# Kernel tuning notes

Hardware: AMD Instinct MI355X
Metric: run time of the kernel (lower is better)

The kernel has to match this reference:

```python
import jax, jax.numpy as jnp
import numpy as np

B, S, D = 2, 2048, 1024
N_HEADS = 16
PAT_HEADS = N_HEADS // 4          # MultiheadAttention num_heads = 4
HEAD_DIM = D // PAT_HEADS         # 256
SPARSITY_RATIO = 0.1
MEMORY_PRESSURE = 0.5
NEG_INF = -1e9


def setup_inputs() -> dict:
    key = jax.random.key(0)
    ks = jax.random.split(key, 16)
    sd = 1.0 / np.sqrt(D)
    sh = 1.0 / np.sqrt(D // 4)
    inp = {
        "q": jax.random.normal(ks[0], (B, S, D), jnp.float32),
        "k": jax.random.normal(ks[1], (B, S, D), jnp.float32),
        "v": jax.random.normal(ks[2], (B, S, D), jnp.float32),
        # sparsity predictor: Linear(D, D//4) -> ReLU -> Linear(D//4, 1) -> Sigmoid
        "w1": jax.random.uniform(ks[3], (D, D // 4), jnp.float32, -sd, sd),
        "b1": jax.random.uniform(ks[4], (D // 4,), jnp.float32, -sd, sd),
        "w2": jax.random.uniform(ks[5], (D // 4, 1), jnp.float32, -sh, sh),
        "b2": jax.random.uniform(ks[6], (1,), jnp.float32, -sh, sh),
        # MultiheadAttention in_proj (split) + out_proj, stored [in, out]
        "wq": jax.random.uniform(ks[7], (D, D), jnp.float32, -sd, sd),
        "bq": jnp.zeros((D,), jnp.float32),
        "wk": jax.random.uniform(ks[8], (D, D), jnp.float32, -sd, sd),
        "bk": jnp.zeros((D,), jnp.float32),
        "wv": jax.random.uniform(ks[9], (D, D), jnp.float32, -sd, sd),
        "bv": jnp.zeros((D,), jnp.float32),
        "wo": jax.random.uniform(ks[10], (D, D), jnp.float32, -sd, sd),
        "bo": jnp.zeros((D,), jnp.float32),
    }
    return inp


def reference(q, k, v, w1, b1, w2, b2, wq, bq, wk, bk, wv, bv, wo, bo):
    # learned importance scores -> boolean mask of active tokens
    h = jax.nn.relu(q @ w1 + b1)                       # [B,S,D//4]
    scores = jax.nn.sigmoid(h @ w2 + b2)[..., 0]       # [B,S]
    threshold = SPARSITY_RATIO * (1.0 + MEMORY_PRESSURE)
    mask = scores > threshold                          # [B,S] bool

    # original module flattens all active tokens across batch into ONE
    # sequence and runs MHA over that subset; we express the identical math
    # with a fixed-shape masked attention over the flattened [B*S] tokens.
    N = B * S
    mf = mask.reshape(N)                               # [N]
    qf = q.reshape(N, D)
    kf = k.reshape(N, D)
    vf = v.reshape(N, D)

    qp = (qf @ wq + bq).reshape(N, PAT_HEADS, HEAD_DIM)
    kp = (kf @ wk + bk).reshape(N, PAT_HEADS, HEAD_DIM)
    vp = (vf @ wv + bv).reshape(N, PAT_HEADS, HEAD_DIM)

    scale = 1.0 / np.sqrt(HEAD_DIM)
    logits = jnp.einsum("nhd,mhd->hnm", qp * scale, kp)   # [H,N,N]
    logits = jnp.where(mf[None, None, :], logits, NEG_INF)  # only active keys
    attn = jax.nn.softmax(logits, axis=-1)
    ctx = jnp.einsum("hnm,mhd->nhd", attn, vp).reshape(N, D)
    out = ctx @ wo + bo                                 # [N,D]

    # scatter back: inactive query positions stay zero
    out = jnp.where(mf[:, None], out, 0.0)
    return out.reshape(B, S, D)
```

## Files before the change

### kernel.cpp

```cpp
#include <hip/hip_runtime.h>
#include <hip/hip_bf16.h>
#include <math.h>

typedef __bf16 bf16x8 __attribute__((ext_vector_type(8)));
typedef __bf16 bf16x4 __attribute__((ext_vector_type(4)));
typedef float  f32x4  __attribute__((ext_vector_type(4)));
typedef float  f32x16 __attribute__((ext_vector_type(16)));
typedef short  s16x8  __attribute__((ext_vector_type(8)));

#define N_TOK  4096
#define DMODEL 1024
#define NHEAD  4
#define DHEAD  256

__device__ __forceinline__ f32x4 mfma16x16(bf16x8 a, bf16x8 b, f32x4 c) {
    return __builtin_amdgcn_mfma_f32_16x16x32_bf16(a, b, c, 0, 0, 0);
}
__device__ __forceinline__ f32x16 mfma32(bf16x8 a, bf16x8 b, f32x16 c) {
    return __builtin_amdgcn_mfma_f32_32x32x16_bf16(a, b, c, 0, 0, 0);
}
__device__ __forceinline__ unsigned cvtpk(float lo, float hi) {
    unsigned r;
    asm("v_cvt_pk_bf16_f32 %0, %1, %2" : "=v"(r) : "v"(lo), "v"(hi));
    return r;
}

__device__ __forceinline__ void gload_lds16(const void* gsrc, void* ldst) {
    __builtin_amdgcn_global_load_lds(
        (const __attribute__((address_space(1))) void*)gsrc,
        (__attribute__((address_space(3))) void*)ldst, 16, 0, 0);
}

struct CvtArgs { const float* src[3]; __bf16* dst[3]; };
__global__ __launch_bounds__(256)
void cvt_bf16_kernel(CvtArgs a)
{
    const float* in = a.src[blockIdx.y];
    __bf16* out = a.dst[blockIdx.y];
    size_t i8 = ((size_t)blockIdx.x * 256 + threadIdx.x) * 8;
    f32x4 t0 = *(const f32x4*)(in + i8);
    f32x4 t1 = *(const f32x4*)(in + i8 + 4);
    bf16x8 b;
    #pragma unroll
    for (int j = 0; j < 4; ++j) { b[j] = (__bf16)t0[j]; b[j + 4] = (__bf16)t1[j]; }
    *(bf16x8*)(out + i8) = b;
}

__device__ __forceinline__ void transposew_body(const float* __restrict__ in,
                                                __bf16* __restrict__ out, int C)
{
    __shared__ __align__(16) __bf16 tile[64 * 72];
    const int tid = threadIdx.x;
    const int r0 = blockIdx.x * 64;
    const int c0 = blockIdx.y * 64;
    if (c0 >= C) return;
    #pragma unroll
    for (int it = 0; it < 4; ++it) {
        int i = tid + it * 256;
        int row = i >> 4, c4 = i & 15;
        f32x4 v = *(const f32x4*)(in + (size_t)(r0 + row) * C + c0 + c4 * 4);
        #pragma unroll
        for (int j = 0; j < 4; ++j)
            tile[(c4 * 4 + j) * 72 + row] = (__bf16)v[j];
    }
    __syncthreads();
    #pragma unroll
    for (int it = 0; it < 2; ++it) {
        int i = tid + it * 256;
        int col = i >> 3, ch = i & 7;
        s16x8 v = *(const s16x8*)(&tile[col * 72 + ch * 8]);
        *(s16x8*)((short*)out + (size_t)(c0 + col) * 1024 + r0 + ch * 8) = v;
    }
}

__global__ __launch_bounds__(256)
void transposew_kernel(const float* __restrict__ in, __bf16* __restrict__ out, int C)
{
    transposew_body(in, out, C);
}

struct TWArgs { const float* src[4]; __bf16* dst[4]; int C[4]; };
__global__ __launch_bounds__(256)
void transposew_batch_kernel(TWArgs a)
{
    int z = blockIdx.z;
    transposew_body(a.src[z], a.dst[z], a.C[z]);
}

struct GemmDesc {
    const __bf16* A; const __bf16* B; const float* bias; __bf16* C;
    int lda, ldb, ldc, gx, nblocks, relu, biasrow; float scale;
};
struct FusedArgs { GemmDesc d[4]; };

__global__ __launch_bounds__(256, 2)
void gemm_fused(FusedArgs fa)
{
    __shared__ __align__(16) short As[2][128 * 64];
    __shared__ __align__(16) short Bs[2][128 * 64];

    int b = blockIdx.x, z = 0;
    while (b >= fa.d[z].nblocks) { b -= fa.d[z].nblocks; ++z; }
    const GemmDesc D = fa.d[z];
    const int m0 = (b % D.gx) * 128;
    const int n0 = (b / D.gx) * 128;

    const int tid  = threadIdx.x;
    const int lane = tid & 63;
    const int wv   = tid >> 6;
    const int c16  = lane & 15;
    const int quad = lane >> 4;
    const int swz  = c16 & 7;
    const int wr   = wv >> 1;
    const int wc   = wv & 1;

    f32x4 acc[4][4];
    #pragma unroll
    for (int i = 0; i < 4; ++i)
        #pragma unroll
        for (int j = 0; j < 4; ++j)
            acc[i][j] = (f32x4){0.f, 0.f, 0.f, 0.f};

    const int sRow = lane >> 3;
    const int sCh  = (lane & 7) ^ (sRow & 7);

    auto issue = [&](short* Abuf, short* Bbuf, int k0) {
        #pragma unroll
        for (int g = 0; g < 4; ++g) {
            int row = 32 * wv + 8 * g + sRow;
            const char* src = (const char*)(D.A + (size_t)(m0 + row) * D.lda + k0) + sCh * 16;
            gload_lds16(src, (char*)Abuf + (32 * wv + 8 * g) * 128);
        }
        #pragma unroll
        for (int g = 0; g < 4; ++g) {
            int row = 32 * wv + 8 * g + sRow;
            const char* src = (const char*)(D.B + (size_t)(n0 + row) * D.ldb + k0) + sCh * 16;
            gload_lds16(src, (char*)Bbuf + (32 * wv + 8 * g) * 128);
        }
    };
    auto compute = [&](const short* Abuf, const short* Bbuf) {
        __builtin_amdgcn_s_setprio(1);
        #pragma unroll
        for (int ks = 0; ks < 2; ++ks) {
            bf16x8 af[4], bfr[4];
            int slot = ((ks * 4 + quad) ^ swz) * 16;
            #pragma unroll
            for (int t = 0; t < 4; ++t)
                af[t] = *(const bf16x8*)((const char*)Abuf + (wr * 64 + t * 16 + c16) * 128 + slot);
            #pragma unroll
            for (int t = 0; t < 4; ++t)
                bfr[t] = *(const bf16x8*)((const char*)Bbuf + (wc * 64 + t * 16 + c16) * 128 + slot);
            #pragma unroll
            for (int tm = 0; tm < 4; ++tm)
                #pragma unroll
                for (int tn = 0; tn < 4; ++tn)
                    acc[tm][tn] = mfma16x16(af[tm], bfr[tn], acc[tm][tn]);
        }
        __builtin_amdgcn_s_setprio(0);
    };

    issue(As[0], Bs[0], 0);
    __syncthreads();

    #pragma unroll 1
    for (int t = 0; t < 16; t += 2) {
        if (t + 1 < 16) issue(As[1], Bs[1], (t + 1) << 6);
        compute(As[0], Bs[0]);
        __syncthreads();
        if (t + 2 < 16) issue(As[0], Bs[0], (t + 2) << 6);
        compute(As[1], Bs[1]);
        __syncthreads();
    }

    #pragma unroll
    for (int tm = 0; tm < 4; ++tm) {
        #pragma unroll
        for (int rr = 0; rr < 4; ++rr) {
            int row = m0 + wr * 64 + tm * 16 + quad * 4 + rr;
            float rbv = D.biasrow ? D.bias[row] : 0.0f;
            #pragma unroll
            for (int tn = 0; tn < 4; ++tn) {
                int col = n0 + wc * 64 + tn * 16 + c16;
                float bb = D.biasrow ? rbv : D.bias[col];
                float val = (acc[tm][tn][rr] + bb) * D.scale;
                if (D.relu) val = fmaxf(val, 0.0f);
                D.C[(size_t)row * D.ldc + col] = (__bf16)val;
            }
        }
    }
}

template<typename OutT, bool BIASROW>
__global__ __launch_bounds__(256, 2)
void gemm_bt64(const __bf16* __restrict__ A, int lda,
               const __bf16* __restrict__ B, int ldb,
               const float* __restrict__ bias,
               OutT* __restrict__ C, int ldc,
               float scale, int relu, const float* __restrict__ rowmask, int K)
{
    __shared__ __align__(16) short As[2][128 * 64];
    __shared__ __align__(16) short Bs[2][64 * 64];
    const int tid  = threadIdx.x;
    const int lane = tid & 63;
    const int wv   = tid >> 6;
    const int c16  = lane & 15;
    const int quad = lane >> 4;
    const int swz  = c16 & 7;
    const int wr   = wv >> 1;
    const int wc   = wv & 1;
    const int m0 = blockIdx.x * 128;
    const int n0 = blockIdx.y * 64;

    f32x4 acc[4][2];
    #pragma unroll
    for (int i = 0; i < 4; ++i)
        #pragma unroll
        for (int j = 0; j < 2; ++j)
            acc[i][j] = (f32x4){0.f, 0.f, 0.f, 0.f};

    const int sRow = lane >> 3;
    const int sCh  = (lane & 7) ^ (sRow & 7);

    auto issue = [&](short* Abuf, short* Bbuf, int k0) {
        #pragma unroll
        for (int g = 0; g < 4; ++g) {
            int row = 32 * wv + 8 * g + sRow;
            const char* src = (const char*)(A + (size_t)(m0 + row) * lda + k0) + sCh * 16;
            gload_lds16(src, (char*)Abuf + (32 * wv + 8 * g) * 128);
        }
        #pragma unroll
        for (int g = 0; g < 2; ++g) {
            int row = 16 * wv + 8 * g + sRow;
            const char* src = (const char*)(B + (size_t)(n0 + row) * ldb + k0) + sCh * 16;
            gload_lds16(src, (char*)Bbuf + (16 * wv + 8 * g) * 128);
        }
    };
    auto compute = [&](const short* Abuf, const short* Bbuf) {
        __builtin_amdgcn_s_setprio(1);
        #pragma unroll
        for (int ks = 0; ks < 2; ++ks) {
            bf16x8 af[4], bfr[2];
            int slot = ((ks * 4 + quad) ^ swz) * 16;
            #pragma unroll
            for (int t = 0; t < 4; ++t)
                af[t] = *(const bf16x8*)((const char*)Abuf + (wr * 64 + t * 16 + c16) * 128 + slot);
            #pragma unroll
            for (int t = 0; t < 2; ++t)
                bfr[t] = *(const bf16x8*)((const char*)Bbuf + (wc * 32 + t * 16 + c16) * 128 + slot);
            #pragma unroll
            for (int tm = 0; tm < 4; ++tm)
                #pragma unroll
                for (int tn = 0; tn < 2; ++tn)
                    acc[tm][tn] = mfma16x16(af[tm], bfr[tn], acc[tm][tn]);
        }
        __builtin_amdgcn_s_setprio(0);
    };

    const int nt = K >> 6;
    issue(As[0], Bs[0], 0);
    __syncthreads();

    #pragma unroll 1
    for (int t = 0; t < nt; t += 2) {
        if (t + 1 < nt) issue(As[1], Bs[1], (t + 1) << 6);
        compute(As[0], Bs[0]);
        __syncthreads();
        if (t + 1 < nt) {
            if (t + 2 < nt) issue(As[0], Bs[0], (t + 2) << 6);
            compute(As[1], Bs[1]);
            __syncthreads();
        }
    }

    #pragma unroll
    for (int tm = 0; tm < 4; ++tm) {
        #pragma unroll
        for (int rr = 0; rr < 4; ++rr) {
            int row = m0 + wr * 64 + tm * 16 + quad * 4 + rr;
            float mk = rowmask ? rowmask[row] : 1.0f;
            float rbv = BIASROW ? bias[row] : 0.0f;
            #pragma unroll
            for (int tn = 0; tn < 2; ++tn) {
                int col = n0 + wc * 32 + tn * 16 + c16;
                float b = BIASROW ? rbv : bias[col];
                float val = (acc[tm][tn][rr] + b) * scale;
                if (relu) val = fmaxf(val, 0.0f);
                val *= mk;
                C[(size_t)row * ldc + col] = (OutT)val;
            }
        }
    }
}

__global__ void score_mask_kernel(const __bf16* __restrict__ h,
                                  const float* __restrict__ w2,
                                  const float* __restrict__ b2,
                                  float* __restrict__ maskf)
{
    int lane = threadIdx.x & 63;
    int tok  = blockIdx.x * 4 + (threadIdx.x >> 6);
    const __bf16* hr = h + (size_t)tok * 256;
    float s = 0.f;
    #pragma unroll
    for (int j = 0; j < 4; ++j) {
        int c = j * 64 + lane;
        s += (float)hr[c] * w2[c];
    }
    #pragma unroll
    for (int o = 1; o < 64; o <<= 1) s += __shfl_xor(s, o);
    if (lane == 0) {
        float x = s + b2[0];
        maskf[tok] = (x > -1.7346010553881064f) ? 1.0f : 0.0f;
    }
}

__global__ __launch_bounds__(512, 1)
void attn_kernel(const __bf16* __restrict__ qp, const __bf16* __restrict__ kp,
                 const __bf16* __restrict__ vpT, const float* __restrict__ maskf,
                 __bf16* __restrict__ O0, __bf16* __restrict__ O1,
                 __bf16* __restrict__ O2, __bf16* __restrict__ O3,
                 float* __restrict__ lbuf)
{
    __shared__ __align__(16) short Ks[2][64 * 256];
    __shared__ __align__(16) short Vs[2][256 * 64];

    const int tid  = threadIdx.x;
    const int lane = tid & 63;
    const int wv   = tid >> 6;
    const int l31  = lane & 31;
    const int hi   = lane >> 5;
    const int swz  = lane & 7;

    const int d    = blockIdx.x;
    const int g    = d & 7;
    const int t    = d >> 3;
    const int head = g >> 1;
    const int ksp  = (g & 1) * 2 + (t >> 4);
    const int qb   = t & 15;
    const int kbase = ksp * 1024;
    const int q0w  = qb * 256 + wv * 32;
    __bf16* Ob = (ksp == 0) ? O0 : (ksp == 1) ? O1 : (ksp == 2) ? O2 : O3;

    bf16x8 qf[16];
    #pragma unroll
    for (int c = 0; c < 16; ++c)
        qf[c] = *(const bf16x8*)(qp + (size_t)(q0w + l31) * DMODEL + head * DHEAD + c * 16 + hi * 8);

    f32x16 o[8];
    #pragma unroll
    for (int i = 0; i < 8; ++i)
        #pragma unroll
        for (int r = 0; r < 16; ++r) o[i][r] = 0.f;
    float ps0 = 0.f, ps1 = 0.f, ps2 = 0.f, ps3 = 0.f;

    const int kRow0 = wv * 8 + (lane >> 5);
    const int kCh   = lane & 31;
    const int vRow0 = wv * 32 + (lane >> 3);
    const int vCh   = (lane & 7) ^ ((lane >> 3) & 7);

    auto issue = [&](int buf, int n0) {
        #pragma unroll
        for (int gg = 0; gg < 4; ++gg) {
            int key = kRow0 + gg * 2;
            int c   = kCh ^ (key & 7);
            const char* src = (const char*)(kp + (size_t)(n0 + key) * DMODEL + head * DHEAD) + c * 16;
            gload_lds16(src, (char*)Ks[buf] + (wv * 8 + gg * 2) * 512);
        }
        #pragma unroll
        for (int gg = 0; gg < 4; ++gg) {
            int row = vRow0 + gg * 8;
            const char* src = (const char*)(vpT + (size_t)(head * DHEAD + row) * N_TOK + n0) + vCh * 16;
            gload_lds16(src, (char*)Vs[buf] + (wv * 32 + gg * 8) * 128);
        }
    };

    issue(0, kbase);
    __syncthreads();
    int cur = 0;

    #pragma unroll 1
    for (int n0 = kbase; n0 < kbase + 1024; n0 += 64) {
        if (n0 + 64 < kbase + 1024) issue(cur ^ 1, n0 + 64);
        const short* Kb = Ks[cur];
        const short* Vb = Vs[cur];

        #pragma unroll
        for (int kb = 0; kb < 2; ++kb) {
            f32x16 s;
            #pragma unroll
            for (int r = 0; r < 16; ++r) s[r] = 0.f;
            __builtin_amdgcn_s_setprio(1);
            #pragma unroll
            for (int c = 0; c < 16; ++c) {
                bf16x8 kf = *(const bf16x8*)((const char*)Kb + (kb * 32 + l31) * 512 + (((c * 2 + hi) ^ swz) << 4));
                s = mfma32(kf, qf[c], s);
            }
            __builtin_amdgcn_s_setprio(0);

            #pragma unroll
            for (int half = 0; half < 2; ++half) {
                float p[8];
                #pragma unroll
                for (int gq = 0; gq < 2; ++gq) {
                    f32x4 mv = *(const f32x4*)(maskf + n0 + kb * 32 + (half * 2 + gq) * 8 + hi * 4);
                    #pragma unroll
                    for (int j = 0; j < 4; ++j) {
                        float pv = __expf(s[(half * 2 + gq) * 4 + j]) * mv[j];
                        p[gq * 4 + j] = pv;
                        if (j == 0) ps0 += pv; else if (j == 1) ps1 += pv;
                        else if (j == 2) ps2 += pv; else ps3 += pv;
                    }
                }
                unsigned A = cvtpk(p[0], p[1]), B = cvtpk(p[2], p[3]);
                unsigned C = cvtpk(p[4], p[5]), D = cvtpk(p[6], p[7]);
                unsigned y0 = (unsigned)__shfl_xor((int)(hi ? A : C), 32);
                unsigned y1 = (unsigned)__shfl_xor((int)(hi ? B : D), 32);
                union { unsigned u[4]; bf16x8 v; } pa;
                pa.u[0] = hi ? y0 : A;  pa.u[1] = hi ? y1 : B;
                pa.u[2] = hi ? C  : y0; pa.u[3] = hi ? D  : y1;
                int chunk = (kb * 2 + half) * 2 + hi;
                __builtin_amdgcn_s_setprio(1);
                #pragma unroll
                for (int dhb = 0; dhb < 8; ++dhb) {
                    bf16x8 vf = *(const bf16x8*)((const char*)Vb + (dhb * 32 + l31) * 128 + ((chunk ^ swz) << 4));
                    o[dhb] = mfma32(pa.v, vf, o[dhb]);
                }
                __builtin_amdgcn_s_setprio(0);
            }
        }
        __syncthreads();
        cur ^= 1;
    }

    float psum = (ps0 + ps1) + (ps2 + ps3);
    float tot = psum + __shfl_xor(psum, 32);
    if (lane < 32)
        lbuf[(size_t)(ksp * NHEAD + head) * N_TOK + q0w + l31] = tot;

    short* Osm = (wv < 4) ? ((short*)Ks + wv * 8192) : ((short*)Vs + (wv - 4) * 8192);
    #pragma unroll
    for (int dhb = 0; dhb < 8; ++dhb)
        #pragma unroll
        for (int r = 0; r < 16; ++r) {
            int qrow = (r & 3) + 8 * (r >> 2) + 4 * hi;
            *(__bf16*)&Osm[qrow * 256 + dhb * 32 + l31] = (__bf16)o[dhb][r];
        }
    __builtin_amdgcn_s_waitcnt(0xc07f);
    #pragma unroll
    for (int j = 0; j < 16; ++j) {
        int row = j * 2 + hi;
        bf16x8 tv = *(const bf16x8*)&Osm[row * 256 + l31 * 8];
        *(bf16x8*)(Ob + (size_t)(q0w + row) * DMODEL + head * DHEAD + l31 * 8) = tv;
    }
}

__global__ void combine_kernel(const __bf16* __restrict__ O0,
                               const __bf16* __restrict__ O1,
                               const __bf16* __restrict__ O2,
                               const __bf16* __restrict__ O3,
                               const float* __restrict__ lbuf,
                               __bf16* __restrict__ out)
{
    int idx  = blockIdx.x * 256 + threadIdx.x;
    int tok  = idx >> 7;
    int g    = idx & 127;
    int head = g >> 5;
    float l0 = lbuf[(size_t)(0 * NHEAD + head) * N_TOK + tok];
    float l1 = lbuf[(size_t)(1 * NHEAD + head) * N_TOK + tok];
    float l2 = lbuf[(size_t)(2 * NHEAD + head) * N_TOK + tok];
    float l3 = lbuf[(size_t)(3 * NHEAD + head) * N_TOK + tok];
    float inv = 1.0f / (l0 + l1 + l2 + l3);
    size_t off = (size_t)tok * DMODEL + g * 8;
    bf16x8 a = *(const bf16x8*)(O0 + off);
    bf16x8 b = *(const bf16x8*)(O1 + off);
    bf16x8 c = *(const bf16x8*)(O2 + off);
    bf16x8 dd = *(const bf16x8*)(O3 + off);
    bf16x8 z;
    #pragma unroll
    for (int j = 0; j < 8; ++j)
        z[j] = (__bf16)((((float)a[j] + (float)b[j]) + ((float)c[j] + (float)dd[j])) * inv);
    *(bf16x8*)(out + off) = z;
}

extern "C" void kernel_launch(void* const* d_in, const int* in_sizes, int n_in,
                              void* d_out, int out_size, void* d_ws, size_t ws_size,
                              hipStream_t stream)
{
    (void)in_sizes; (void)n_in; (void)out_size;
    const float* q  = (const float*)d_in[0];
    const float* k  = (const float*)d_in[1];
    const float* v  = (const float*)d_in[2];
    const float* w1 = (const float*)d_in[3];
    const float* b1 = (const float*)d_in[4];
    const float* w2 = (const float*)d_in[5];
    const float* b2 = (const float*)d_in[6];
    const float* wq = (const float*)d_in[7];
    const float* bq = (const float*)d_in[8];
    const float* wk = (const float*)d_in[9];
    const float* bk = (const float*)d_in[10];
    const float* wvw = (const float*)d_in[11];
    const float* bv = (const float*)d_in[12];
    const float* wo = (const float*)d_in[13];
    const float* bo = (const float*)d_in[14];

    if (ws_size < 35667968u + 8388608u + 131072u) return;

    char* ws = (char*)d_ws;
    float*  maskf = (float*)ws;
    __bf16* hbuf  = (__bf16*)(ws + 16384);
    float*  lbuf  = (float*)(ws + 16384);
    __bf16* qp    = (__bf16*)(ws + 16384 + 2097152);
    __bf16* kpb   = qp  + 4194304;
    __bf16* vpT   = kpb + 4194304;
    __bf16* ctx   = vpT + 4194304;
    __bf16* O1    = (__bf16*)(ws + 35667968u);

    __bf16* wqT = (__bf16*)d_out;
    __bf16* wkT = wqT + 1048576;
    __bf16* wvT = wkT + 1048576;
    __bf16* w1T = wvT + 1048576;
    __bf16* vbf = (__bf16*)((char*)d_out + 6815744u);
    __bf16* O2  = (__bf16*)d_out;
    __bf16* O3  = (__bf16*)((char*)d_out + 8388608u);
    __bf16* woT = hbuf;
    __bf16* qbf = O1;
    __bf16* kbf = ctx;

    CvtArgs ca;
    ca.src[0] = q;  ca.dst[0] = qbf;
    ca.src[1] = k;  ca.dst[1] = kbf;
    ca.src[2] = v;  ca.dst[2] = vbf;
    cvt_bf16_kernel<<<dim3(2048, 3), 256, 0, stream>>>(ca);

    TWArgs ta;
    ta.src[0] = w1;  ta.dst[0] = w1T;  ta.C[0] = 256;
    ta.src[1] = wq;  ta.dst[1] = wqT;  ta.C[1] = 1024;
    ta.src[2] = wk;  ta.dst[2] = wkT;  ta.C[2] = 1024;
    ta.src[3] = wvw; ta.dst[3] = wvT;  ta.C[3] = 1024;
    transposew_batch_kernel<<<dim3(16, 16, 4), 256, 0, stream>>>(ta);

    FusedArgs fa;
    fa.d[0] = { qbf, w1T, b1, hbuf, 1024, 1024,  256, 32,  64, 1, 0, 1.0f };
    fa.d[1] = { qbf, wqT, bq, qp,   1024, 1024, 1024, 32, 256, 0, 0, 0.0625f };
    fa.d[2] = { kbf, wkT, bk, kpb,  1024, 1024, 1024, 32, 256, 0, 0, 1.0f };
    fa.d[3] = { wvT, vbf, bv, vpT,  1024, 1024, 4096,  8, 256, 0, 1, 1.0f };
    gemm_fused<<<dim3(832), 256, 0, stream>>>(fa);

    score_mask_kernel<<<1024, 256, 0, stream>>>(hbuf, w2, b2, maskf);

    attn_kernel<<<dim3(256), 512, 0, stream>>>(qp, kpb, vpT, maskf, ctx, O1, O2, O3, lbuf);
    combine_kernel<<<2048, 256, 0, stream>>>(ctx, O1, O2, O3, lbuf, ctx);

    transposew_kernel<<<dim3(16, 16), 256, 0, stream>>>(wo, woT, 1024);
    gemm_bt64<float, false><<<dim3(32, 16), 256, 0, stream>>>(
        ctx, 1024, woT, 1024, bo, (float*)d_out, 1024, 1.0f, 0, maskf, 1024);
}
```

Measured before the change: 374.9 us.

## Remap blocks to XCDs and halve attention key-split with 256-thread blocks

The fused projection GEMM and output GEMM now assign block indices so that each XCD (blockIdx mod 8) works on a contiguous range of M rows, which should improve L2 reuse of shared A tiles. The attention kernel drops from a 4-way to a 2-way key split. It uses 256-thread blocks covering 128 queries each, with each wave loading twice as many K/V rows per stage, and the combine kernel merges only two partials. This cuts partial-output traffic and combine work, but each block now walks a longer key loop with fewer waves, which lowers latency hiding per CU.

```diff
diff --git a/kernel.cpp b/kernel.cpp
--- a/kernel.cpp
+++ b/kernel.cpp
@@ -89,7 +89,7 @@
 
 struct GemmDesc {
     const __bf16* A; const __bf16* B; const float* bias; __bf16* C;
-    int lda, ldb, ldc, gx, nblocks, relu, biasrow; float scale;
+    int lda, ldb, ldc, relu, biasrow; float scale;
 };
 struct FusedArgs { GemmDesc d[4]; };
 
@@ -99,11 +99,26 @@
     __shared__ __align__(16) short As[2][128 * 64];
     __shared__ __align__(16) short Bs[2][128 * 64];
 
-    int b = blockIdx.x, z = 0;
-    while (b >= fa.d[z].nblocks) { b -= fa.d[z].nblocks; ++z; }
+    const int dd  = blockIdx.x;
+    const int xcd = dd & 7;
+    const int slot = dd >> 3;
+    int z, mIdx, nIdx;
+    if (slot < 8) {
+        z = 0; int s = slot;
+        mIdx = xcd * 4 + (s >> 1); nIdx = s & 1;
+    } else if (slot < 40) {
+        z = 1; int s = slot - 8;
+        mIdx = xcd * 4 + (s >> 3); nIdx = s & 7;
+    } else if (slot < 72) {
+        z = 2; int s = slot - 40;
+        mIdx = xcd * 4 + (s >> 3); nIdx = s & 7;
+    } else {
+        z = 3; int s = slot - 72;
+        nIdx = xcd * 4 + (s >> 3); mIdx = s & 7;
+    }
     const GemmDesc D = fa.d[z];
-    const int m0 = (b % D.gx) * 128;
-    const int n0 = (b / D.gx) * 128;
+    const int m0 = mIdx * 128;
+    const int n0 = nIdx * 128;
 
     const int tid  = threadIdx.x;
     const int lane = tid & 63;
@@ -143,13 +158,13 @@
         #pragma unroll
         for (int ks = 0; ks < 2; ++ks) {
             bf16x8 af[4], bfr[4];
-            int slot = ((ks * 4 + quad) ^ swz) * 16;
+            int slot2 = ((ks * 4 + quad) ^ swz) * 16;
             #pragma unroll
             for (int t = 0; t < 4; ++t)
-                af[t] = *(const bf16x8*)((const char*)Abuf + (wr * 64 + t * 16 + c16) * 128 + slot);
+                af[t] = *(const bf16x8*)((const char*)Abuf + (wr * 64 + t * 16 + c16) * 128 + slot2);
             #pragma unroll
             for (int t = 0; t < 4; ++t)
-                bfr[t] = *(const bf16x8*)((const char*)Bbuf + (wc * 64 + t * 16 + c16) * 128 + slot);
+                bfr[t] = *(const bf16x8*)((const char*)Bbuf + (wc * 64 + t * 16 + c16) * 128 + slot2);
             #pragma unroll
             for (int tm = 0; tm < 4; ++tm)
                 #pragma unroll
@@ -190,16 +205,22 @@
     }
 }
 
-template<typename OutT, bool BIASROW>
+template<typename OutT>
 __global__ __launch_bounds__(256, 2)
-void gemm_bt64(const __bf16* __restrict__ A, int lda,
-               const __bf16* __restrict__ B, int ldb,
-               const float* __restrict__ bias,
-               OutT* __restrict__ C, int ldc,
-               float scale, int relu, const float* __restrict__ rowmask, int K)
+void gemm_out(const __bf16* __restrict__ A, int lda,
+              const __bf16* __restrict__ B, int ldb,
+              const float* __restrict__ bias,
+              OutT* __restrict__ C, int ldc,
+              float scale, const float* __restrict__ rowmask, int K)
 {
     __shared__ __align__(16) short As[2][128 * 64];
     __shared__ __align__(16) short Bs[2][64 * 64];
+    const int dd  = blockIdx.x;
+    const int xcd = dd & 7;
+    const int s   = dd >> 3;
+    const int m0  = (xcd * 4 + (s >> 4)) * 128;
+    const int n0  = (s & 15) * 64;
+
     const int tid  = threadIdx.x;
     const int lane = tid & 63;
     const int wv   = tid >> 6;
@@ -208,8 +229,6 @@
     const int swz  = c16 & 7;
     const int wr   = wv >> 1;
     const int wc   = wv & 1;
-    const int m0 = blockIdx.x * 128;
-    const int n0 = blockIdx.y * 64;
 
     f32x4 acc[4][2];
     #pragma unroll
@@ -278,13 +297,10 @@
         for (int rr = 0; rr < 4; ++rr) {
             int row = m0 + wr * 64 + tm * 16 + quad * 4 + rr;
             float mk = rowmask ? rowmask[row] : 1.0f;
-            float rbv = BIASROW ? bias[row] : 0.0f;
             #pragma unroll
             for (int tn = 0; tn < 2; ++tn) {
                 int col = n0 + wc * 32 + tn * 16 + c16;
-                float b = BIASROW ? rbv : bias[col];
-                float val = (acc[tm][tn][rr] + b) * scale;
-                if (relu) val = fmaxf(val, 0.0f);
+                float val = (acc[tm][tn][rr] + bias[col]) * scale;
                 val *= mk;
                 C[(size_t)row * ldc + col] = (OutT)val;
             }
@@ -314,11 +330,10 @@
     }
 }
 
-__global__ __launch_bounds__(512, 1)
+__global__ __launch_bounds__(256, 1)
 void attn_kernel(const __bf16* __restrict__ qp, const __bf16* __restrict__ kp,
                  const __bf16* __restrict__ vpT, const float* __restrict__ maskf,
                  __bf16* __restrict__ O0, __bf16* __restrict__ O1,
-                 __bf16* __restrict__ O2, __bf16* __restrict__ O3,
                  float* __restrict__ lbuf)
 {
     __shared__ __align__(16) short Ks[2][64 * 256];
@@ -332,14 +347,14 @@
     const int swz  = lane & 7;
 
     const int d    = blockIdx.x;
-    const int g    = d & 7;
-    const int t    = d >> 3;
-    const int head = g >> 1;
-    const int ksp  = (g & 1) * 2 + (t >> 4);
-    const int qb   = t & 15;
-    const int kbase = ksp * 1024;
-    const int q0w  = qb * 256 + wv * 32;
-    __bf16* Ob = (ksp == 0) ? O0 : (ksp == 1) ? O1 : (ksp == 2) ? O2 : O3;
+    const int orig = ((d & 7) << 5) | (d >> 3);
+    const int qb   = orig & 31;
+    const int head = (orig >> 5) & 3;
+    const int ksp  = orig >> 7;
+    const int kbase = ksp * 2048;
+    const int kend  = kbase + 2048;
+    const int q0w  = qb * 128 + wv * 32;
+    __bf16* Ob = ksp ? O1 : O0;
 
     bf16x8 qf[16];
     #pragma unroll
@@ -353,24 +368,24 @@
         for (int r = 0; r < 16; ++r) o[i][r] = 0.f;
     float ps0 = 0.f, ps1 = 0.f, ps2 = 0.f, ps3 = 0.f;
 
-    const int kRow0 = wv * 8 + (lane >> 5);
+    const int kRow0 = wv * 16 + (lane >> 5);
     const int kCh   = lane & 31;
-    const int vRow0 = wv * 32 + (lane >> 3);
+    const int vRow0 = wv * 64 + (lane >> 3);
     const int vCh   = (lane & 7) ^ ((lane >> 3) & 7);
 
     auto issue = [&](int buf, int n0) {
         #pragma unroll
-        for (int gg = 0; gg < 4; ++gg) {
+        for (int gg = 0; gg < 8; ++gg) {
             int key = kRow0 + gg * 2;
             int c   = kCh ^ (key & 7);
             const char* src = (const char*)(kp + (size_t)(n0 + key) * DMODEL + head * DHEAD) + c * 16;
-            gload_lds16(src, (char*)Ks[buf] + (wv * 8 + gg * 2) * 512);
-        }
-        #pragma unroll
-        for (int gg = 0; gg < 4; ++gg) {
+            gload_lds16(src, (char*)Ks[buf] + (wv * 16 + gg * 2) * 512);
+        }
+        #pragma unroll
+        for (int gg = 0; gg < 8; ++gg) {
             int row = vRow0 + gg * 8;
             const char* src = (const char*)(vpT + (size_t)(head * DHEAD + row) * N_TOK + n0) + vCh * 16;
-            gload_lds16(src, (char*)Vs[buf] + (wv * 32 + gg * 8) * 128);
+            gload_lds16(src, (char*)Vs[buf] + (wv * 64 + gg * 8) * 128);
         }
     };
 
@@ -379,8 +394,8 @@
     int cur = 0;
 
     #pragma unroll 1
-    for (int n0 = kbase; n0 < kbase + 1024; n0 += 64) {
-        if (n0 + 64 < kbase + 1024) issue(cur ^ 1, n0 + 64);
+    for (int n0 = kbase; n0 < kend; n0 += 64) {
+        if (n0 + 64 < kend) issue(cur ^ 1, n0 + 64);
         const short* Kb = Ks[cur];
         const short* Vb = Vs[cur];
 
@@ -437,7 +452,7 @@
     if (lane < 32)
         lbuf[(size_t)(ksp * NHEAD + head) * N_TOK + q0w + l31] = tot;
 
-    short* Osm = (wv < 4) ? ((short*)Ks + wv * 8192) : ((short*)Vs + (wv - 4) * 8192);
+    short* Osm = (short*)Ks + wv * 8192;
     #pragma unroll
     for (int dhb = 0; dhb < 8; ++dhb)
         #pragma unroll
@@ -456,8 +471,6 @@
 
 __global__ void combine_kernel(const __bf16* __restrict__ O0,
                                const __bf16* __restrict__ O1,
-                               const __bf16* __restrict__ O2,
-                               const __bf16* __restrict__ O3,
                                const float* __restrict__ lbuf,
                                __bf16* __restrict__ out)
 {
@@ -465,20 +478,16 @@
     int tok  = idx >> 7;
     int g    = idx & 127;
     int head = g >> 5;
-    float l0 = lbuf[(size_t)(0 * NHEAD + head) * N_TOK + tok];
-    float l1 = lbuf[(size_t)(1 * NHEAD + head) * N_TOK + tok];
-    float l2 = lbuf[(size_t)(2 * NHEAD + head) * N_TOK + tok];
-    float l3 = lbuf[(size_t)(3 * NHEAD + head) * N_TOK + tok];
-    float inv = 1.0f / (l0 + l1 + l2 + l3);
+    float a = lbuf[(size_t)head * N_TOK + tok];
+    float b = lbuf[(size_t)(NHEAD + head) * N_TOK + tok];
+    float inv = 1.0f / (a + b);
     size_t off = (size_t)tok * DMODEL + g * 8;
-    bf16x8 a = *(const bf16x8*)(O0 + off);
-    bf16x8 b = *(const bf16x8*)(O1 + off);
-    bf16x8 c = *(const bf16x8*)(O2 + off);
-    bf16x8 dd = *(const bf16x8*)(O3 + off);
+    bf16x8 x = *(const bf16x8*)(O0 + off);
+    bf16x8 y = *(const bf16x8*)(O1 + off);
     bf16x8 z;
     #pragma unroll
     for (int j = 0; j < 8; ++j)
-        z[j] = (__bf16)((((float)a[j] + (float)b[j]) + ((float)c[j] + (float)dd[j])) * inv);
+        z[j] = (__bf16)(((float)x[j] + (float)y[j]) * inv);
     *(bf16x8*)(out + off) = z;
 }
 
@@ -508,20 +517,18 @@
     char* ws = (char*)d_ws;
     float*  maskf = (float*)ws;
     __bf16* hbuf  = (__bf16*)(ws + 16384);
-    float*  lbuf  = (float*)(ws + 16384);
     __bf16* qp    = (__bf16*)(ws + 16384 + 2097152);
     __bf16* kpb   = qp  + 4194304;
     __bf16* vpT   = kpb + 4194304;
     __bf16* ctx   = vpT + 4194304;
     __bf16* O1    = (__bf16*)(ws + 35667968u);
+    float*  lbuf  = (float*)(ws + 35667968u + 8388608u);
 
     __bf16* wqT = (__bf16*)d_out;
     __bf16* wkT = wqT + 1048576;
     __bf16* wvT = wkT + 1048576;
     __bf16* w1T = wvT + 1048576;
     __bf16* vbf = (__bf16*)((char*)d_out + 6815744u);
-    __bf16* O2  = (__bf16*)d_out;
-    __bf16* O3  = (__bf16*)((char*)d_out + 8388608u);
     __bf16* woT = hbuf;
     __bf16* qbf = O1;
     __bf16* kbf = ctx;
@@ -540,18 +547,18 @@
     transposew_batch_kernel<<<dim3(16, 16, 4), 256, 0, stream>>>(ta);
 
     FusedArgs fa;
-    fa.d[0] = { qbf, w1T, b1, hbuf, 1024, 1024,  256, 32,  64, 1, 0, 1.0f };
-    fa.d[1] = { qbf, wqT, bq, qp,   1024, 1024, 1024, 32, 256, 0, 0, 0.0625f };
-    fa.d[2] = { kbf, wkT, bk, kpb,  1024, 1024, 1024, 32, 256, 0, 0, 1.0f };
-    fa.d[3] = { wvT, vbf, bv, vpT,  1024, 1024, 4096,  8, 256, 0, 1, 1.0f };
+    fa.d[0] = { qbf, w1T, b1, hbuf, 1024, 1024,  256, 1, 0, 1.0f };
+    fa.d[1] = { qbf, wqT, bq, qp,   1024, 1024, 1024, 0, 0, 0.0625f };
+    fa.d[2] = { kbf, wkT, bk, kpb,  1024, 1024, 1024, 0, 0, 1.0f };
+    fa.d[3] = { wvT, vbf, bv, vpT,  1024, 1024, 4096, 0, 1, 1.0f };
     gemm_fused<<<dim3(832), 256, 0, stream>>>(fa);
 
     score_mask_kernel<<<1024, 256, 0, stream>>>(hbuf, w2, b2, maskf);
-
-    attn_kernel<<<dim3(256), 512, 0, stream>>>(qp, kpb, vpT, maskf, ctx, O1, O2, O3, lbuf);
-    combine_kernel<<<2048, 256, 0, stream>>>(ctx, O1, O2, O3, lbuf, ctx);
-
     transposew_kernel<<<dim3(16, 16), 256, 0, stream>>>(wo, woT, 1024);
-    gemm_bt64<float, false><<<dim3(32, 16), 256, 0, stream>>>(
-        ctx, 1024, woT, 1024, bo, (float*)d_out, 1024, 1.0f, 0, maskf, 1024);
-}
+
+    attn_kernel<<<dim3(256), 256, 0, stream>>>(qp, kpb, vpT, maskf, ctx, O1, lbuf);
+    combine_kernel<<<2048, 256, 0, stream>>>(ctx, O1, lbuf, ctx);
+
+    gemm_out<float><<<dim3(512), 256, 0, stream>>>(
+        ctx, 1024, woT, 1024, bo, (float*)d_out, 1024, 1.0f, maskf, 1024);
+}
```

New measurement: 330.9 us. -11.7%, faster.
